# Kernel optimization log

Measured on AMD Instinct MI355X. Metric: run time of the kernel, lower is better.

The kernel has to match this reference:

```python
import math
import jax, jax.numpy as jnp
import numpy as np

D_MODEL = 512
D_K = 64


def setup_inputs() -> dict:
    key = jax.random.key(0)
    k1, k2, k3, k4 = jax.random.split(key, 4)
    x = jax.random.normal(k1, (4, 4096, D_MODEL), dtype=jnp.float32)
    s = 1.0 / math.sqrt(D_MODEL)
    # torch nn.Linear weights have shape (out_features, in_features)
    W_Q = jax.random.uniform(k2, (D_K, D_MODEL), jnp.float32, -s, s)
    W_K = jax.random.uniform(k3, (D_K, D_MODEL), jnp.float32, -s, s)
    W_V = jax.random.uniform(k4, (D_K, D_MODEL), jnp.float32, -s, s)
    return {"x": x, "W_Q": W_Q, "W_K": W_K, "W_V": W_V}


def reference(x, W_Q, W_K, W_V):
    d_k = W_Q.shape[0]
    # Q,K,V: (B,S,d_k) via x @ W.T (torch Linear convention)
    Q = jnp.einsum('bsd,kd->bsk', x, W_Q)
    K = jnp.einsum('bsd,kd->bsk', x, W_K)
    V = jnp.einsum('bsd,kd->bsk', x, W_V)
    scores = jnp.einsum('bqk,bsk->bqs', Q, K) / math.sqrt(d_k)  # (B,S,S)
    S = x.shape[1]
    causal_mask = jnp.triu(jnp.ones((S, S), dtype=bool), k=1)
    scores = jnp.where(causal_mask[None], -jnp.inf, scores)
    attn = jax.nn.softmax(scores, axis=-1)
    return jnp.einsum('bqs,bsk->bqk', attn, V)
```

## Files before the change

kernel.cpp:

```cpp
#include <hip/hip_runtime.h>
#include <hip/hip_bf16.h>
#include <math.h>

typedef short short4v __attribute__((ext_vector_type(4)));
typedef short short8 __attribute__((ext_vector_type(8)));
typedef __bf16 bf16x8 __attribute__((ext_vector_type(8)));
typedef float f32x4 __attribute__((ext_vector_type(4)));

#define SEQ 4096
#define QK_SCALE 0.18033688011112042f

__device__ __forceinline__ short f2bf(float f) {
    __bf16 h = (__bf16)f;
    return __builtin_bit_cast(short, h);
}

__device__ __forceinline__ float exp2a(float x) {
    float r;
    asm("v_exp_f32 %0, %1" : "=v"(r) : "v"(x));
    return r;
}

__device__ __forceinline__ f32x4 mfma16(short8 a, short8 b, f32x4 c) {
    return __builtin_amdgcn_mfma_f32_16x16x32_bf16(
        __builtin_bit_cast(bf16x8, a), __builtin_bit_cast(bf16x8, b), c, 0, 0, 0);
}

__global__ __launch_bounds__(256) void wconv_kernel(
    const float* __restrict__ wq, const float* __restrict__ wk,
    const float* __restrict__ wv, short* __restrict__ out) {
  int i = blockIdx.x * 256 + threadIdx.x;
  const int j = i & 7, lane = (i >> 3) & 63, nb = (i >> 9) & 3;
  const int t = (i >> 11) & 15, mat = i >> 15;
  const int g = lane >> 4, r = lane & 15;
  const int src = (nb * 16 + r) * 512 + t * 32 + g * 8 + j;
  float v;
  if (mat == 0)      v = wq[src] * QK_SCALE;
  else if (mat == 1) v = wk[src];
  else               v = wv[src];
  out[i] = f2bf(v);
}

__global__ __launch_bounds__(256) void proj_kernel(
    const float* __restrict__ x, const short* __restrict__ wf,
    short* __restrict__ Qs, short* __restrict__ Ks, short* __restrict__ Vt) {
  __shared__ short stg[4][16][72];
  const int bb = blockIdx.x;
  const int mat = bb >> 8, rb = bb & 255;
  const int wave = threadIdx.x >> 6, lane = threadIdx.x & 63;
  const int g = lane >> 4, r = lane & 15;
  const int rbase = rb * 64 + wave * 16;
  const short* wbase = wf + (size_t)mat * 32768;

  f32x4 acc[4];
#pragma unroll
  for (int nb = 0; nb < 4; ++nb) acc[nb] = (f32x4)0.f;

  const float* xp = x + (size_t)(rbase + r) * 512;
#pragma unroll 4
  for (int k0 = 0; k0 < 512; k0 += 32) {
    const int kb = k0 + g * 8;
    f32x4 f0 = *(const f32x4*)(xp + kb);
    f32x4 f1 = *(const f32x4*)(xp + kb + 4);
    short8 a;
    a[0] = f2bf(f0[0]); a[1] = f2bf(f0[1]); a[2] = f2bf(f0[2]); a[3] = f2bf(f0[3]);
    a[4] = f2bf(f1[0]); a[5] = f2bf(f1[1]); a[6] = f2bf(f1[2]); a[7] = f2bf(f1[3]);
    const short* wp = wbase + ((size_t)(k0 >> 5) * 4 * 64 + lane) * 8;
#pragma unroll
    for (int nb = 0; nb < 4; ++nb) {
      short8 bq = *(const short8*)(wp + nb * 512);
      acc[nb] = mfma16(a, bq, acc[nb]);
    }
  }

#pragma unroll
  for (int nb = 0; nb < 4; ++nb) {
#pragma unroll
    for (int reg = 0; reg < 4; ++reg)
      stg[wave][g * 4 + reg][nb * 16 + r] = f2bf(acc[nb][reg]);
  }
  if (mat < 2) {
    short* dst = (mat == 0) ? Qs : Ks;
    const int orow = lane >> 2, ob = lane & 3;
    short8 v0 = *(const short8*)&stg[wave][orow][ob * 8];
    short8 v1 = *(const short8*)&stg[wave][orow][ob * 8 + 32];
    *(short8*)(dst + (size_t)(rbase + orow) * 64 + ob * 8) = v0;
    *(short8*)(dst + (size_t)(rbase + orow) * 64 + ob * 8 + 32) = v1;
  } else {
    const int b = rbase >> 12, sb = rbase & 4095;
    short* vrow = Vt + ((size_t)(b * 64 + lane)) * SEQ + sb;
    short8 v0, v1;
#pragma unroll
    for (int j = 0; j < 8; ++j) v0[j] = stg[wave][j][lane];
#pragma unroll
    for (int j = 0; j < 8; ++j) v1[j] = stg[wave][j + 8][lane];
    *(short8*)(vrow) = v0;
    *(short8*)(vrow + 8) = v1;
  }
}

__global__ __launch_bounds__(256) void attn_kernel(
    const short* __restrict__ Qs, const short* __restrict__ Ks,
    const short* __restrict__ Vt, float* __restrict__ out) {
  __shared__ __align__(16) short ptq[4][2][16][80];
  __shared__ __align__(16) float po[4][32][68];
  __shared__ float pm[4][32], pl[4][32];
  const int blk = blockIdx.x;
  const int b = blk & 3;
  const int t = 127 - (blk >> 2);
  const int wave = threadIdx.x >> 6, lane = threadIdx.x & 63;
  const int g = lane >> 4, r = lane & 15;
  const int qbase = t * 32;
  const short* Qb = Qs + (size_t)b * (SEQ * 64);
  const short* Kb = Ks + (size_t)b * (SEQ * 64);
  const short* Vb = Vt + (size_t)b * (64 * SEQ);

  short8 qf[2][2];
#pragma unroll
  for (int rb = 0; rb < 2; ++rb) {
    const int qoff = (qbase + rb * 16 + r) * 64 + g * 8;
    qf[rb][0] = *(const short8*)(Qb + qoff);
    qf[rb][1] = *(const short8*)(Qb + qoff + 32);
  }

  f32x4 o[2][4];
  float m[2] = {-1e30f, -1e30f}, l[2] = {0.f, 0.f};
#pragma unroll
  for (int rb = 0; rb < 2; ++rb)
#pragma unroll
    for (int nb = 0; nb < 4; ++nb) o[rb][nb] = (f32x4)0.f;

  for (int s0 = wave * 64; s0 <= qbase + 31; s0 += 256) {
    short8 kf0[4], kf1[4];
#pragma unroll
    for (int nc = 0; nc < 4; ++nc) {
      const int koff = (s0 + nc * 16 + r) * 64 + g * 8;
      kf0[nc] = *(const short8*)(Kb + koff);
      kf1[nc] = *(const short8*)(Kb + koff + 32);
    }
    short8 vv0[4], vv1[4];
#pragma unroll
    for (int nb = 0; nb < 4; ++nb) {
      const int voff = (nb * 16 + r) * SEQ + s0 + g * 8;
      vv0[nb] = *(const short8*)(Vb + voff);
      vv1[nb] = *(const short8*)(Vb + voff + 32);
    }

#pragma unroll
    for (int rb = 0; rb < 2; ++rb) {
      f32x4 sc[4];
#pragma unroll
      for (int nc = 0; nc < 4; ++nc) {
        sc[nc] = (f32x4)0.f;
        sc[nc] = mfma16(kf0[nc], qf[rb][0], sc[nc]);
        sc[nc] = mfma16(kf1[nc], qf[rb][1], sc[nc]);
      }
      const int q = qbase + rb * 16 + r;
      if (s0 + 63 > q) {
#pragma unroll
        for (int nc = 0; nc < 4; ++nc) {
          const int sbase = s0 + nc * 16 + g * 4;
#pragma unroll
          for (int reg = 0; reg < 4; ++reg)
            if (sbase + reg > q) sc[nc][reg] = -1e30f;
        }
      }
      float mx = fmaxf(fmaxf(sc[0][0], sc[0][1]), fmaxf(sc[0][2], sc[0][3]));
#pragma unroll
      for (int nc = 1; nc < 4; ++nc)
        mx = fmaxf(mx, fmaxf(fmaxf(sc[nc][0], sc[nc][1]), fmaxf(sc[nc][2], sc[nc][3])));
      mx = fmaxf(mx, __shfl_xor(mx, 16));
      mx = fmaxf(mx, __shfl_xor(mx, 32));
      const float mn = fmaxf(m[rb], mx);
      const float fac = exp2a(m[rb] - mn);
      m[rb] = mn;
      float rs = 0.f;
#pragma unroll
      for (int nc = 0; nc < 4; ++nc) {
#pragma unroll
        for (int reg = 0; reg < 4; ++reg) {
          const float p = exp2a(sc[nc][reg] - mn);
          sc[nc][reg] = p;
          rs += p;
        }
      }
      rs += __shfl_xor(rs, 16);
      rs += __shfl_xor(rs, 32);
      l[rb] = l[rb] * fac + rs;
#pragma unroll
      for (int nb = 0; nb < 4; ++nb) o[rb][nb] *= fac;
#pragma unroll
      for (int nc = 0; nc < 4; ++nc) {
        short4v p4;
        p4[0] = f2bf(sc[nc][0]); p4[1] = f2bf(sc[nc][1]);
        p4[2] = f2bf(sc[nc][2]); p4[3] = f2bf(sc[nc][3]);
        *(short4v*)&ptq[wave][rb][r][nc * 16 + g * 4] = p4;
      }
      const short8 pa0 = *(const short8*)&ptq[wave][rb][r][g * 8];
      const short8 pa1 = *(const short8*)&ptq[wave][rb][r][32 + g * 8];
#pragma unroll
      for (int nb = 0; nb < 4; ++nb) {
        o[rb][nb] = mfma16(vv0[nb], pa0, o[rb][nb]);
        o[rb][nb] = mfma16(vv1[nb], pa1, o[rb][nb]);
      }
    }
  }

#pragma unroll
  for (int rb = 0; rb < 2; ++rb) {
#pragma unroll
    for (int nb = 0; nb < 4; ++nb)
      *(f32x4*)&po[wave][rb * 16 + r][nb * 16 + g * 4] = o[rb][nb];
    if (g == 0) {
      pm[wave][rb * 16 + r] = m[rb];
      pl[wave][rb * 16 + r] = l[rb];
    }
  }
  __syncthreads();
  {
    const int tid = threadIdx.x;
    const int row = tid >> 3, cb = (tid & 7) * 8;
    float M = fmaxf(fmaxf(pm[0][row], pm[1][row]), fmaxf(pm[2][row], pm[3][row]));
    float scw[4], L = 0.f;
#pragma unroll
    for (int w = 0; w < 4; ++w) {
      scw[w] = exp2a(pm[w][row] - M);
      L += pl[w][row] * scw[w];
    }
    const float inv = 1.f / L;
    f32x4 acc0 = (f32x4)0.f, acc1 = (f32x4)0.f;
#pragma unroll
    for (int w = 0; w < 4; ++w) {
      const f32x4 a = *(const f32x4*)&po[w][row][cb];
      const f32x4 c = *(const f32x4*)&po[w][row][cb + 4];
      acc0 += a * scw[w];
      acc1 += c * scw[w];
    }
    acc0 *= inv; acc1 *= inv;
    float* op = out + ((size_t)b * SEQ + qbase + row) * 64 + cb;
    *(f32x4*)op = acc0;
    *(f32x4*)(op + 4) = acc1;
  }
}

extern "C" void kernel_launch(void* const* d_in, const int* in_sizes, int n_in,
                              void* d_out, int out_size, void* d_ws, size_t ws_size,
                              hipStream_t stream) {
  (void)in_sizes; (void)n_in; (void)out_size; (void)ws_size;
  const float* x  = (const float*)d_in[0];
  const float* wq = (const float*)d_in[1];
  const float* wk = (const float*)d_in[2];
  const float* wv = (const float*)d_in[3];
  float* out = (float*)d_out;

  short* ws  = (short*)d_ws;
  short* wbf = ws;
  short* Qs  = ws + 98304;
  short* Ks  = Qs + 1048576;
  short* Vt  = Ks + 1048576;

  wconv_kernel<<<384, 256, 0, stream>>>(wq, wk, wv, wbf);
  proj_kernel<<<768, 256, 0, stream>>>(x, wbf, Qs, Ks, Vt);
  attn_kernel<<<512, 256, 0, stream>>>(Qs, Ks, Vt, out);
}
```

Measured before the change: 140.8 us.

## Split attention KV range across eight waves with aliased shared memory

```diff
diff --git a/kernel.cpp b/kernel.cpp
--- a/kernel.cpp
+++ b/kernel.cpp
@@ -99,15 +99,15 @@
   }
 }
 
-__global__ __launch_bounds__(256) void attn_kernel(
+#define REGION 8960
+__global__ __launch_bounds__(512, 4) void attn_kernel(
     const short* __restrict__ Qs, const short* __restrict__ Ks,
     const short* __restrict__ Vt, float* __restrict__ out) {
-  __shared__ __align__(16) short ptq[4][2][16][80];
-  __shared__ __align__(16) float po[4][32][68];
-  __shared__ float pm[4][32], pl[4][32];
+  __shared__ __align__(16) char smem[8][REGION];
   const int blk = blockIdx.x;
-  const int b = blk & 3;
-  const int t = 127 - (blk >> 2);
+  const int c = blk & 255, k = blk >> 8;
+  const int t = k ? (c >> 1) : (127 - (c >> 1));
+  const int b = (k << 1) | (c & 1);
   const int wave = threadIdx.x >> 6, lane = threadIdx.x & 63;
   const int g = lane >> 4, r = lane & 15;
   const int qbase = t * 32;
@@ -115,6 +115,11 @@
   const short* Kb = Ks + (size_t)b * (SEQ * 64);
   const short* Vb = Vt + (size_t)b * (64 * SEQ);
 
+  short* ptq_w = (short*)smem[wave];
+  float* po_w  = (float*)smem[wave];
+  float* pm_w  = (float*)(smem[wave] + 8704);
+  float* pl_w  = (float*)(smem[wave] + 8832);
+
   short8 qf[2][2];
 #pragma unroll
   for (int rb = 0; rb < 2; ++rb) {
@@ -130,7 +135,7 @@
 #pragma unroll
     for (int nb = 0; nb < 4; ++nb) o[rb][nb] = (f32x4)0.f;
 
-  for (int s0 = wave * 64; s0 <= qbase + 31; s0 += 256) {
+  for (int s0 = wave * 64; s0 <= qbase + 31; s0 += 512) {
     short8 kf0[4], kf1[4];
 #pragma unroll
     for (int nc = 0; nc < 4; ++nc) {
@@ -194,10 +199,10 @@
         short4v p4;
         p4[0] = f2bf(sc[nc][0]); p4[1] = f2bf(sc[nc][1]);
         p4[2] = f2bf(sc[nc][2]); p4[3] = f2bf(sc[nc][3]);
-        *(short4v*)&ptq[wave][rb][r][nc * 16 + g * 4] = p4;
-      }
-      const short8 pa0 = *(const short8*)&ptq[wave][rb][r][g * 8];
-      const short8 pa1 = *(const short8*)&ptq[wave][rb][r][32 + g * 8];
+        *(short4v*)(ptq_w + rb * 1280 + r * 80 + nc * 16 + g * 4) = p4;
+      }
+      const short8 pa0 = *(const short8*)(ptq_w + rb * 1280 + r * 80 + g * 8);
+      const short8 pa1 = *(const short8*)(ptq_w + rb * 1280 + r * 80 + 32 + g * 8);
 #pragma unroll
       for (int nb = 0; nb < 4; ++nb) {
         o[rb][nb] = mfma16(vv0[nb], pa0, o[rb][nb]);
@@ -206,40 +211,38 @@
     }
   }
 
+  asm volatile("s_waitcnt lgkmcnt(0)" ::: "memory");
 #pragma unroll
   for (int rb = 0; rb < 2; ++rb) {
 #pragma unroll
     for (int nb = 0; nb < 4; ++nb)
-      *(f32x4*)&po[wave][rb * 16 + r][nb * 16 + g * 4] = o[rb][nb];
+      *(f32x4*)(po_w + (size_t)(rb * 16 + r) * 68 + nb * 16 + g * 4) = o[rb][nb];
     if (g == 0) {
-      pm[wave][rb * 16 + r] = m[rb];
-      pl[wave][rb * 16 + r] = l[rb];
+      pm_w[rb * 16 + r] = m[rb];
+      pl_w[rb * 16 + r] = l[rb];
     }
   }
   __syncthreads();
   {
     const int tid = threadIdx.x;
-    const int row = tid >> 3, cb = (tid & 7) * 8;
-    float M = fmaxf(fmaxf(pm[0][row], pm[1][row]), fmaxf(pm[2][row], pm[3][row]));
-    float scw[4], L = 0.f;
-#pragma unroll
-    for (int w = 0; w < 4; ++w) {
-      scw[w] = exp2a(pm[w][row] - M);
-      L += pl[w][row] * scw[w];
+    const int row = tid >> 4, cb = (tid & 15) * 4;
+    float M = -1e30f;
+#pragma unroll
+    for (int w = 0; w < 8; ++w)
+      M = fmaxf(M, *(const float*)(smem[w] + 8704 + row * 4));
+    float scw[8], L = 0.f;
+#pragma unroll
+    for (int w = 0; w < 8; ++w) {
+      scw[w] = exp2a(*(const float*)(smem[w] + 8704 + row * 4) - M);
+      L += *(const float*)(smem[w] + 8832 + row * 4) * scw[w];
     }
     const float inv = 1.f / L;
-    f32x4 acc0 = (f32x4)0.f, acc1 = (f32x4)0.f;
-#pragma unroll
-    for (int w = 0; w < 4; ++w) {
-      const f32x4 a = *(const f32x4*)&po[w][row][cb];
-      const f32x4 c = *(const f32x4*)&po[w][row][cb + 4];
-      acc0 += a * scw[w];
-      acc1 += c * scw[w];
-    }
-    acc0 *= inv; acc1 *= inv;
-    float* op = out + ((size_t)b * SEQ + qbase + row) * 64 + cb;
-    *(f32x4*)op = acc0;
-    *(f32x4*)(op + 4) = acc1;
+    f32x4 acc = (f32x4)0.f;
+#pragma unroll
+    for (int w = 0; w < 8; ++w)
+      acc += *(const f32x4*)((const float*)smem[w] + (size_t)row * 68 + cb) * scw[w];
+    acc *= inv;
+    *(f32x4*)(out + ((size_t)b * SEQ + qbase + row) * 64 + cb) = acc;
   }
 }
 
@@ -261,5 +264,5 @@
 
   wconv_kernel<<<384, 256, 0, stream>>>(wq, wk, wv, wbf);
   proj_kernel<<<768, 256, 0, stream>>>(x, wbf, Qs, Ks, Vt);
-  attn_kernel<<<512, 256, 0, stream>>>(Qs, Ks, Vt, out);
-}
+  attn_kernel<<<512, 512, 0, stream>>>(Qs, Ks, Vt, out);
+}
```

Measured after the change: 168.4 us. 19.6% more time.
